# Performance work log

Measured on AMD Instinct MI355X. Metric: run time of the kernel, lower is better.

## Reference

```python
import jax, jax.numpy as jnp
import numpy as np


def _get_mask(in_features, out_features, in_flow_features, mask_type=None):
    # Faithful port of the torch get_mask() used by MADE.
    if mask_type == 'input':
        in_degrees = np.arange(in_features) % in_flow_features
    else:
        in_degrees = np.arange(in_features) % (in_flow_features - 1)
    if mask_type == 'output':
        out_degrees = np.arange(out_features) % in_flow_features - 1
    else:
        out_degrees = np.arange(out_features) % (in_flow_features - 1)
    return jnp.asarray((out_degrees[:, None] >= in_degrees[None, :]).astype(np.float32))


def setup_inputs() -> dict:
    B, D, H = 8192, 128, 2048
    key = jax.random.key(0)
    ks = jax.random.split(key, 7)
    w_scale_in = 1.0 / np.sqrt(D)
    w_scale_h = 1.0 / np.sqrt(H)
    return {
        'inputs': jax.random.normal(ks[0], (B, D), dtype=jnp.float32),
        's_w0': jax.random.normal(ks[1], (H, D), dtype=jnp.float32) * w_scale_in,
        's_b0': jnp.zeros((H,), dtype=jnp.float32),
        's_w1': jax.random.normal(ks[2], (H, H), dtype=jnp.float32) * w_scale_h,
        's_b1': jnp.zeros((H,), dtype=jnp.float32),
        's_w2': jax.random.normal(ks[3], (D, H), dtype=jnp.float32) * w_scale_h,
        's_b2': jnp.zeros((D,), dtype=jnp.float32),
        't_w0': jax.random.normal(ks[4], (H, D), dtype=jnp.float32) * w_scale_in,
        't_b0': jnp.zeros((H,), dtype=jnp.float32),
        't_w1': jax.random.normal(ks[5], (H, H), dtype=jnp.float32) * w_scale_h,
        't_b1': jnp.zeros((H,), dtype=jnp.float32),
        't_w2': jax.random.normal(ks[6], (D, H), dtype=jnp.float32) * w_scale_h,
        't_b2': jnp.zeros((D,), dtype=jnp.float32),
    }


def reference(inputs, s_w0, s_b0, s_w1, s_b1, s_w2, s_b2,
              t_w0, t_b0, t_w1, t_b1, t_w2, t_b2):
    # MADESplit forward, mode='direct', num_cond_inputs=None, pre_exp_tanh=False.
    D = inputs.shape[1]
    H = s_w0.shape[0]
    m_in = _get_mask(D, H, D, 'input')    # [H, D]
    m_h = _get_mask(H, H, D)              # [H, H]
    m_out = _get_mask(H, D, D, 'output')  # [D, H]

    def masked_mlp(w0, b0, w1, b1, w2, b2, act):
        h = act(inputs @ (m_in * w0).T + b0)   # joiner + first trunk activation
        h = act(h @ (m_h * w1).T + b1)
        return h @ (m_out * w2).T + b2

    m = masked_mlp(s_w0, s_b0, s_w1, s_b1, s_w2, s_b2, jnp.tanh)
    a = masked_mlp(t_w0, t_b0, t_w1, t_b1, t_w2, t_b2, jax.nn.relu)
    u = (inputs - m) * jnp.exp(-a)
    return u, -a.sum(-1, keepdims=True)
```

## Files before the change

kernel.cpp:

```cpp
#include <hip/hip_runtime.h>
#include <hip/hip_bf16.h>

typedef unsigned short u16;
typedef __attribute__((ext_vector_type(8))) short bf16x8;
typedef __attribute__((ext_vector_type(4))) float f32x4;

constexpr int NB = 8192, ND = 128, NH = 2048;

__device__ __forceinline__ u16 f2bf(float x) {
  union { float f; unsigned u; } v; v.f = x;
  unsigned r = v.u + 0x7fffu + ((v.u >> 16) & 1u);
  return (u16)(r >> 16);
}
__device__ __forceinline__ float bf2f(u16 h) {
  union { unsigned u; float f; } v; v.u = ((unsigned)h) << 16; return v.f;
}
__device__ __forceinline__ void store_split(u16* hi, u16* lo, long i, float v) {
  u16 h = f2bf(v);
  hi[i] = h;
  lo[i] = f2bf(v - bf2f(h));
}

__device__ __forceinline__ int deg_sorted(int j) {
  return (j < 272) ? (j / 17) : ((j - 16) >> 4);
}
__device__ __forceinline__ int perm_h(int j) {
  int g, r;
  if (j < 272) { g = j / 17; r = j - g * 17; }
  else         { g = (j - 16) >> 4; r = (j - 16) & 15; }
  return g + 127 * r;
}
__device__ __forceinline__ int offset_of_deg(int g) {
  return (g < 16) ? 17 * g : 16 * g + 16;
}

__device__ __forceinline__ void gll16(const u16* g, u16* l) {
  __builtin_amdgcn_global_load_lds(
      (const __attribute__((address_space(1))) unsigned*)g,
      (__attribute__((address_space(3))) unsigned*)l, 16, 0, 0);
}

__device__ __forceinline__ f32x4 mfma_bb(bf16x8 a, bf16x8 b, f32x4 c) {
  return __builtin_amdgcn_mfma_f32_16x16x32_bf16(a, b, c, 0, 0, 0);
}

template <int PHASE>
__global__ void prep_all(const float* __restrict__ x,
                         const float* __restrict__ w0, const float* __restrict__ b0,
                         const float* __restrict__ w1, const float* __restrict__ b1,
                         const float* __restrict__ w2,
                         u16* __restrict__ xhi, u16* __restrict__ xlo,
                         u16* __restrict__ w0hi, u16* __restrict__ w0lo,
                         u16* __restrict__ w1hi, u16* __restrict__ w1lo,
                         u16* __restrict__ w2hi, u16* __restrict__ w2lo,
                         float* __restrict__ b0p, float* __restrict__ b1p) {
  constexpr int XB  = (NB * ND) / 256;
  constexpr int W0B = (NH * ND) / 256;
  constexpr int W1B = (NH * NH) / 256;
  constexpr int W2B = (ND * NH) / 256;
  constexpr int BB  = NH / 256;
  int bid = blockIdx.x;
  const int tid = threadIdx.x;

  if (PHASE == 0) {
    if (bid < XB) {
      long i = (long)bid * 256 + tid;
      store_split(xhi, xlo, i, x[i]);
      return;
    }
    bid -= XB;
  }
  if (bid < W0B) {
    int i = bid * 256 + tid;
    int r_out = i >> 7, c = i & 127;
    float v = (deg_sorted(r_out) >= c) ? w0[perm_h(r_out) * ND + c] : 0.0f;
    store_split(w0hi, w0lo, i, v);
    return;
  }
  bid -= W0B;
  if (bid < W1B) {
    long i = (long)bid * 256 + tid;
    int r_out = (int)(i >> 11), c_out = (int)(i & 2047);
    float v = (deg_sorted(r_out) >= deg_sorted(c_out))
                  ? w1[(long)perm_h(r_out) * NH + perm_h(c_out)] : 0.0f;
    store_split(w1hi, w1lo, i, v);
    return;
  }
  bid -= W1B;
  if (bid < W2B) {
    int i = bid * 256 + tid;
    int r = i >> 11, c_out = i & 2047;
    float v = ((r - 1) >= deg_sorted(c_out)) ? w2[(r << 11) + perm_h(c_out)] : 0.0f;
    store_split(w2hi, w2lo, i, v);
    return;
  }
  bid -= W2B;
  if (bid < BB) { int j = bid * 256 + tid; b0p[j] = b0[perm_h(j)]; return; }
  bid -= BB;
  { int j = bid * 256 + tid; b1p[j] = b1[perm_h(j)]; }
}

template <int ACT, int BOUND>
__global__ __launch_bounds__(256, 2) void gemm_split(
    const u16* __restrict__ Ahi, const u16* __restrict__ Alo,
    const u16* __restrict__ Bhi, const u16* __restrict__ Blo,
    const float* __restrict__ bias,
    u16* __restrict__ Chi, u16* __restrict__ Clo,
    float* __restrict__ Cf,
    int M, int N, int K, int ksteps_arg) {
  const int tid = threadIdx.x;
  const int l = tid & 63;
  const int w = tid >> 6;
  const int wr = w >> 1, wc = w & 1;
  const int bm = blockIdx.y * 128;
  const int ntile = gridDim.x - 1 - blockIdx.x;
  const int bn = ntile * 128;
  int ksteps;
  if (BOUND == 1) {
    int ghi = deg_sorted(bn + 127);
    ksteps = (ghi + 1 + 31) >> 5;
  } else if (BOUND == 2) {
    int ghi = deg_sorted(bn + 127);
    ksteps = (offset_of_deg(ghi + 1) + 31) >> 5;
  } else {
    ksteps = ksteps_arg;
  }
  const long kbase = (long)blockIdx.z * ksteps * 32;

  __shared__ __align__(16) u16 sAhi[4096];
  __shared__ __align__(16) u16 sAlo[4096];
  __shared__ __align__(16) u16 sBhi[4096];
  __shared__ __align__(16) u16 sBlo[4096];

  f32x4 acc[4][4] = {};

  const int srow = tid >> 2;
  const int scol = (tid & 3) << 3;
  const long aOff0 = (long)(bm + srow) * K + scol + kbase;
  const long aOff1 = aOff0 + 64L * K;
  const long bOff0 = (long)(bn + srow) * K + scol + kbase;
  const long bOff1 = bOff0 + 64L * K;
  const int ldst0 = tid * 8;
  const int ldst1 = 2048 + tid * 8;

  const int fr = l & 15, fq = l >> 4;

  for (int ks = 0; ks < ksteps; ++ks) {
    const long kk = (long)ks * 32;
    __syncthreads();
    gll16(Ahi + aOff0 + kk, sAhi + ldst0);
    gll16(Ahi + aOff1 + kk, sAhi + ldst1);
    gll16(Alo + aOff0 + kk, sAlo + ldst0);
    gll16(Alo + aOff1 + kk, sAlo + ldst1);
    gll16(Bhi + bOff0 + kk, sBhi + ldst0);
    gll16(Bhi + bOff1 + kk, sBhi + ldst1);
    gll16(Blo + bOff0 + kk, sBlo + ldst0);
    gll16(Blo + bOff1 + kk, sBlo + ldst1);
    __syncthreads();

    bf16x8 ah[4], alo[4], bh[4], blo[4];
#pragma unroll
    for (int m = 0; m < 4; ++m) {
      const int off = (wr * 64 + m * 16 + fr) * 32 + fq * 8;
      ah[m]  = *(const bf16x8*)(sAhi + off);
      alo[m] = *(const bf16x8*)(sAlo + off);
    }
#pragma unroll
    for (int n = 0; n < 4; ++n) {
      const int off = (wc * 64 + n * 16 + fr) * 32 + fq * 8;
      bh[n]  = *(const bf16x8*)(sBhi + off);
      blo[n] = *(const bf16x8*)(sBlo + off);
    }
#pragma unroll
    for (int m = 0; m < 4; ++m)
#pragma unroll
      for (int n = 0; n < 4; ++n) {
        acc[m][n] = mfma_bb(ah[m],  bh[n],  acc[m][n]);
        acc[m][n] = mfma_bb(alo[m], bh[n],  acc[m][n]);
        acc[m][n] = mfma_bb(ah[m],  blo[n], acc[m][n]);
      }
  }

  if (ACT == 2) {
    float* out = Cf + (long)blockIdx.z * M * N;
#pragma unroll
    for (int m = 0; m < 4; ++m) {
      const int row = bm + wr * 64 + m * 16 + fq * 4;
#pragma unroll
      for (int n = 0; n < 4; ++n) {
        const int col = bn + wc * 64 + n * 16 + fr;
#pragma unroll
        for (int r = 0; r < 4; ++r)
          out[(long)(row + r) * N + col] = acc[m][n][r];
      }
    }
  } else {
#pragma unroll
    for (int m = 0; m < 4; ++m) {
      const int row = bm + wr * 64 + m * 16 + fq * 4;
#pragma unroll
      for (int n = 0; n < 4; ++n) {
        const int col = bn + wc * 64 + n * 16 + fr;
        const float bv = bias[col];
#pragma unroll
        for (int r = 0; r < 4; ++r) {
          float z = acc[m][n][r] + bv;
          float h = (ACT == 0) ? tanhf(z) : fmaxf(z, 0.0f);
          long idx = (long)(row + r) * N + col;
          store_split(Chi, Clo, idx, h);
        }
      }
    }
  }
}

__global__ void finalize_kernel(const float* __restrict__ x,
                                const float* __restrict__ pm,
                                const float* __restrict__ pa,
                                const float* __restrict__ sb2,
                                const float* __restrict__ tb2,
                                float* __restrict__ out_u,
                                float* __restrict__ out_s) {
  const int b = blockIdx.x * 4 + (threadIdx.x >> 6);
  const int l = threadIdx.x & 63;
  const long base = (long)b * 128;
  float m0 = sb2[l], m1 = sb2[64 + l];
  float a0 = tb2[l], a1 = tb2[64 + l];
#pragma unroll
  for (int k = 0; k < 4; ++k) {
    const long o = (long)k * ((long)NB * ND) + base;
    m0 += pm[o + l];      m1 += pm[o + 64 + l];
    a0 += pa[o + l];      a1 += pa[o + 64 + l];
  }
  out_u[base + l]      = (x[base + l]      - m0) * expf(-a0);
  out_u[base + 64 + l] = (x[base + 64 + l] - m1) * expf(-a1);
  float s = a0 + a1;
#pragma unroll
  for (int off = 32; off; off >>= 1) s += __shfl_down(s, off);
  if (l == 0) out_s[b] = -s;
}

extern "C" void kernel_launch(void* const* d_in, const int* in_sizes, int n_in,
                              void* d_out, int out_size, void* d_ws, size_t ws_size,
                              hipStream_t stream) {
  (void)in_sizes; (void)n_in; (void)out_size; (void)ws_size;
  const float* x   = (const float*)d_in[0];
  const float* sw0 = (const float*)d_in[1];
  const float* sb0 = (const float*)d_in[2];
  const float* sw1 = (const float*)d_in[3];
  const float* sb1 = (const float*)d_in[4];
  const float* sw2 = (const float*)d_in[5];
  const float* sb2 = (const float*)d_in[6];
  const float* tw0 = (const float*)d_in[7];
  const float* tb0 = (const float*)d_in[8];
  const float* tw1 = (const float*)d_in[9];
  const float* tb1 = (const float*)d_in[10];
  const float* tw2 = (const float*)d_in[11];
  const float* tb2 = (const float*)d_in[12];

  char* ws = (char*)d_ws;
  size_t off = 0;
  auto alloc = [&](size_t bytes) {
    void* p = ws + off;
    off += (bytes + 255) & ~(size_t)255;
    return p;
  };
  u16* xhi  = (u16*)alloc((size_t)NB * ND * 2);
  u16* xlo  = (u16*)alloc((size_t)NB * ND * 2);
  u16* w0hi = (u16*)alloc((size_t)NH * ND * 2);
  u16* w0lo = (u16*)alloc((size_t)NH * ND * 2);
  u16* w1hi = (u16*)alloc((size_t)NH * NH * 2);
  u16* w1lo = (u16*)alloc((size_t)NH * NH * 2);
  u16* w2hi = (u16*)alloc((size_t)ND * NH * 2);
  u16* w2lo = (u16*)alloc((size_t)ND * NH * 2);
  u16* h1hi = (u16*)alloc((size_t)NB * NH * 2);
  u16* h1lo = (u16*)alloc((size_t)NB * NH * 2);
  u16* h2hi = (u16*)alloc((size_t)NB * NH * 2);
  u16* h2lo = (u16*)alloc((size_t)NB * NH * 2);
  float* pm  = (float*)alloc((size_t)4 * NB * ND * 4);
  float* pa  = (float*)alloc((size_t)4 * NB * ND * 4);
  float* b0p = (float*)alloc((size_t)NH * 4);
  float* b1p = (float*)alloc((size_t)NH * 4);

  float* out_u = (float*)d_out;
  float* out_s = out_u + (long)NB * ND;

  constexpr int XB  = (NB * ND) / 256;
  constexpr int WSEG = (NH * ND) / 256 + (NH * NH) / 256 + (ND * NH) / 256 + 2 * (NH / 256);

  auto run_mlp = [&](int phase, const float* w0, const float* b0, const float* w1,
                     const float* b1, const float* w2, float* part, bool is_tanh) {
    if (phase == 0)
      prep_all<0><<<XB + WSEG, 256, 0, stream>>>(x, w0, b0, w1, b1, w2,
                                                 xhi, xlo, w0hi, w0lo, w1hi, w1lo,
                                                 w2hi, w2lo, b0p, b1p);
    else
      prep_all<1><<<WSEG, 256, 0, stream>>>(x, w0, b0, w1, b1, w2,
                                            xhi, xlo, w0hi, w0lo, w1hi, w1lo,
                                            w2hi, w2lo, b0p, b1p);
    dim3 g12(NH / 128, NB / 128, 1);
    if (is_tanh) {
      gemm_split<0, 1><<<g12, 256, 0, stream>>>(xhi, xlo, w0hi, w0lo, b0p,
                                                h1hi, h1lo, nullptr, NB, NH, ND, 0);
      gemm_split<0, 2><<<g12, 256, 0, stream>>>(h1hi, h1lo, w1hi, w1lo, b1p,
                                                h2hi, h2lo, nullptr, NB, NH, NH, 0);
    } else {
      gemm_split<1, 1><<<g12, 256, 0, stream>>>(xhi, xlo, w0hi, w0lo, b0p,
                                                h1hi, h1lo, nullptr, NB, NH, ND, 0);
      gemm_split<1, 2><<<g12, 256, 0, stream>>>(h1hi, h1lo, w1hi, w1lo, b1p,
                                                h2hi, h2lo, nullptr, NB, NH, NH, 0);
    }
    dim3 g3(1, NB / 128, 4);
    gemm_split<2, 0><<<g3, 256, 0, stream>>>(h2hi, h2lo, w2hi, w2lo, nullptr,
                                             nullptr, nullptr, part, NB, ND, NH,
                                             (NH / 4) / 32);
  };

  run_mlp(0, sw0, sb0, sw1, sb1, sw2, pm, true);
  run_mlp(1, tw0, tb0, tw1, tb1, tw2, pa, false);

  finalize_kernel<<<NB / 4, 256, 0, stream>>>(x, pm, pa, sb2, tb2, out_u, out_s);
}
```

Before: 609.9 us.

## Stage weight rows in shared memory for permuted prep; interleave tiles; raise occupancy

```diff
diff --git a/kernel.cpp b/kernel.cpp
--- a/kernel.cpp
+++ b/kernel.cpp
@@ -45,20 +45,14 @@
 }
 
 template <int PHASE>
-__global__ void prep_all(const float* __restrict__ x,
-                         const float* __restrict__ w0, const float* __restrict__ b0,
-                         const float* __restrict__ w1, const float* __restrict__ b1,
-                         const float* __restrict__ w2,
-                         u16* __restrict__ xhi, u16* __restrict__ xlo,
-                         u16* __restrict__ w0hi, u16* __restrict__ w0lo,
-                         u16* __restrict__ w1hi, u16* __restrict__ w1lo,
-                         u16* __restrict__ w2hi, u16* __restrict__ w2lo,
-                         float* __restrict__ b0p, float* __restrict__ b1p) {
+__global__ void prep_small(const float* __restrict__ x,
+                           const float* __restrict__ w0,
+                           const float* __restrict__ b0, const float* __restrict__ b1,
+                           u16* __restrict__ xhi, u16* __restrict__ xlo,
+                           u16* __restrict__ w0hi, u16* __restrict__ w0lo,
+                           float* __restrict__ b0p, float* __restrict__ b1p) {
   constexpr int XB  = (NB * ND) / 256;
   constexpr int W0B = (NH * ND) / 256;
-  constexpr int W1B = (NH * NH) / 256;
-  constexpr int W2B = (ND * NH) / 256;
-  constexpr int BB  = NH / 256;
   int bid = blockIdx.x;
   const int tid = threadIdx.x;
 
@@ -78,30 +72,46 @@
     return;
   }
   bid -= W0B;
-  if (bid < W1B) {
-    long i = (long)bid * 256 + tid;
-    int r_out = (int)(i >> 11), c_out = (int)(i & 2047);
-    float v = (deg_sorted(r_out) >= deg_sorted(c_out))
-                  ? w1[(long)perm_h(r_out) * NH + perm_h(c_out)] : 0.0f;
-    store_split(w1hi, w1lo, i, v);
-    return;
-  }
-  bid -= W1B;
-  if (bid < W2B) {
-    int i = bid * 256 + tid;
-    int r = i >> 11, c_out = i & 2047;
-    float v = ((r - 1) >= deg_sorted(c_out)) ? w2[(r << 11) + perm_h(c_out)] : 0.0f;
-    store_split(w2hi, w2lo, i, v);
-    return;
-  }
-  bid -= W2B;
-  if (bid < BB) { int j = bid * 256 + tid; b0p[j] = b0[perm_h(j)]; return; }
-  bid -= BB;
-  { int j = bid * 256 + tid; b1p[j] = b1[perm_h(j)]; }
+  if (bid < 8) { int j = bid * 256 + tid; b0p[j] = b0[perm_h(j)]; return; }
+  { int j = (bid - 8) * 256 + tid; b1p[j] = b1[perm_h(j)]; }
+}
+
+__global__ void prep_rows(const float* __restrict__ w1, const float* __restrict__ w2,
+                          u16* __restrict__ w1hi, u16* __restrict__ w1lo,
+                          u16* __restrict__ w2hi, u16* __restrict__ w2lo) {
+  __shared__ float row[NH];
+  const int j = blockIdx.x;
+  const int tid = threadIdx.x;
+  const float* src = (j < NH) ? (w1 + (long)perm_h(j) * NH)
+                              : (w2 + (long)(j - NH) * NH);
+  const float4* s4 = (const float4*)src;
+  float4* r4 = (float4*)row;
+#pragma unroll
+  for (int i = 0; i < 2; ++i) r4[tid + i * 256] = s4[tid + i * 256];
+  __syncthreads();
+  if (j < NH) {
+    const int dj = deg_sorted(j);
+    const long base = (long)j * NH;
+#pragma unroll
+    for (int k = 0; k < 8; ++k) {
+      int c = k * 256 + tid;
+      float v = (dj >= deg_sorted(c)) ? row[perm_h(c)] : 0.0f;
+      store_split(w1hi, w1lo, base + c, v);
+    }
+  } else {
+    const int r = j - NH;
+    const long base = (long)r * NH;
+#pragma unroll
+    for (int k = 0; k < 8; ++k) {
+      int c = k * 256 + tid;
+      float v = ((r - 1) >= deg_sorted(c)) ? row[perm_h(c)] : 0.0f;
+      store_split(w2hi, w2lo, base + c, v);
+    }
+  }
 }
 
 template <int ACT, int BOUND>
-__global__ __launch_bounds__(256, 2) void gemm_split(
+__global__ __launch_bounds__(256, 3) void gemm_split(
     const u16* __restrict__ Ahi, const u16* __restrict__ Alo,
     const u16* __restrict__ Bhi, const u16* __restrict__ Blo,
     const float* __restrict__ bias,
@@ -113,7 +123,9 @@
   const int w = tid >> 6;
   const int wr = w >> 1, wc = w & 1;
   const int bm = blockIdx.y * 128;
-  const int ntile = gridDim.x - 1 - blockIdx.x;
+  const int NT = gridDim.x;
+  const int bx = blockIdx.x;
+  const int ntile = (bx & 1) ? (bx >> 1) : (NT - 1 - (bx >> 1));
   const int bn = ntile * 128;
   int ksteps;
   if (BOUND == 1) {
@@ -285,19 +297,18 @@
   float* out_u = (float*)d_out;
   float* out_s = out_u + (long)NB * ND;
 
-  constexpr int XB  = (NB * ND) / 256;
-  constexpr int WSEG = (NH * ND) / 256 + (NH * NH) / 256 + (ND * NH) / 256 + 2 * (NH / 256);
+  constexpr int XB   = (NB * ND) / 256;
+  constexpr int WSEG = (NH * ND) / 256 + 2 * (NH / 256);
 
   auto run_mlp = [&](int phase, const float* w0, const float* b0, const float* w1,
                      const float* b1, const float* w2, float* part, bool is_tanh) {
     if (phase == 0)
-      prep_all<0><<<XB + WSEG, 256, 0, stream>>>(x, w0, b0, w1, b1, w2,
-                                                 xhi, xlo, w0hi, w0lo, w1hi, w1lo,
-                                                 w2hi, w2lo, b0p, b1p);
+      prep_small<0><<<XB + WSEG, 256, 0, stream>>>(x, w0, b0, b1, xhi, xlo,
+                                                   w0hi, w0lo, b0p, b1p);
     else
-      prep_all<1><<<WSEG, 256, 0, stream>>>(x, w0, b0, w1, b1, w2,
-                                            xhi, xlo, w0hi, w0lo, w1hi, w1lo,
-                                            w2hi, w2lo, b0p, b1p);
+      prep_small<1><<<WSEG, 256, 0, stream>>>(x, w0, b0, b1, xhi, xlo,
+                                              w0hi, w0lo, b0p, b1p);
+    prep_rows<<<NH + ND, 256, 0, stream>>>(w1, w2, w1hi, w1lo, w2hi, w2lo);
     dim3 g12(NH / 128, NB / 128, 1);
     if (is_tanh) {
       gemm_split<0, 1><<<g12, 256, 0, stream>>>(xhi, xlo, w0hi, w0lo, b0p,
```

Result: no change. 601.7 us (-1.3%).
